# Kernel tuning notes

Measured on AMD Instinct MI355X. Metric: run time of the kernel, lower is better.

## Reference

```python
import jax, jax.numpy as jnp
import numpy as np

TEMPERATURE = 0.07
MASK_VALUE = -10000.0
EPS = 1e-12  # matches F.normalize eps


def setup_inputs() -> dict:
    key = jax.random.key(0)
    k1, k2 = jax.random.split(key)
    B, D = 8192, 512
    embeddings = jax.random.normal(k1, (B, D), dtype=jnp.float32)
    positive_mask = jax.random.randint(k2, (B, B), 0, 2).astype(bool)
    return {"embeddings": embeddings, "positive_mask": positive_mask}


def reference(embeddings, positive_mask):
    B = embeddings.shape[0]
    # L2 normalize rows (F.normalize with eps clamp)
    norm = jnp.maximum(jnp.linalg.norm(embeddings, axis=1, keepdims=True), EPS)
    e = embeddings / norm
    sim = jnp.matmul(e, e.T) / TEMPERATURE  # (B, B)
    eye = jnp.eye(B, dtype=bool)
    sim = jnp.where(eye, MASK_VALUE, sim)
    pos = positive_mask & ~eye
    counts = pos.sum(axis=1)  # (B,)
    pos_sum = jnp.sum(jnp.where(pos, sim, 0.0), axis=1)  # (B,)
    lse = jax.nn.logsumexp(sim, axis=1)  # (B,)
    pos_mean = pos_sum / jnp.maximum(counts, 1).astype(sim.dtype)
    # rows with positives: -mean(pos) + lse; rows without: just lse
    row_loss = jnp.where(counts > 0, lse - pos_mean, lse)
    return jnp.mean(row_loss)
```

## Files before the change

### kernel.cpp

```cpp
#include <hip/hip_runtime.h>
#include <hip/hip_bf16.h>

#define BN_ 8192
#define DK_ 512
#define TEMP_INV 14.2857142857142857f
#define LOG2E_ 1.44269504088896f
#define MAXOFF 15.0f

typedef __bf16 bf16x8 __attribute__((ext_vector_type(8)));
typedef float f32x4 __attribute__((ext_vector_type(4)));

__device__ inline unsigned short f2bf(float f) {
    unsigned u = __float_as_uint(f);
    return (unsigned short)((u + 0x7FFFu + ((u >> 16) & 1u)) >> 16);
}

__global__ __launch_bounds__(256) void norm_kernel(const float* __restrict__ emb,
                                                   unsigned short* __restrict__ ebf) {
    const int row  = blockIdx.x * 4 + (threadIdx.x >> 6);
    const int lane = threadIdx.x & 63;
    const float4* src = reinterpret_cast<const float4*>(emb + (size_t)row * DK_);
    float4 v0 = src[lane];
    float4 v1 = src[lane + 64];
    float ss = v0.x*v0.x + v0.y*v0.y + v0.z*v0.z + v0.w*v0.w
             + v1.x*v1.x + v1.y*v1.y + v1.z*v1.z + v1.w*v1.w;
#pragma unroll
    for (int off = 1; off < 64; off <<= 1) ss += __shfl_xor(ss, off, 64);
    const float scale = 1.0f / fmaxf(sqrtf(ss), 1e-12f);
    uint2 o0, o1;
    o0.x = (unsigned)f2bf(v0.x * scale) | ((unsigned)f2bf(v0.y * scale) << 16);
    o0.y = (unsigned)f2bf(v0.z * scale) | ((unsigned)f2bf(v0.w * scale) << 16);
    o1.x = (unsigned)f2bf(v1.x * scale) | ((unsigned)f2bf(v1.y * scale) << 16);
    o1.y = (unsigned)f2bf(v1.z * scale) | ((unsigned)f2bf(v1.w * scale) << 16);
    uint2* dst = reinterpret_cast<uint2*>(ebf + (size_t)row * DK_);
    dst[lane]      = o0;
    dst[lane + 64] = o1;
}

__global__ __launch_bounds__(256, 4) void infonce_main(
    const unsigned short* __restrict__ ebf,
    const int* __restrict__ mask,
    float* __restrict__ se, float* __restrict__ ps, float* __restrict__ ct) {

    __shared__ unsigned short As[128 * 64];
    __shared__ unsigned short Bs[128 * 64];
    __shared__ unsigned char  pmB[128 * 16];
    __shared__ float red2[2][128];

    const int t    = threadIdx.x;
    const int lane = t & 63;
    const int wid  = t >> 6;
    const int wr   = wid >> 1;
    const int wc   = wid & 1;
    const int rb   = blockIdx.x;
    const int cb   = blockIdx.y;

    if (t < 128) { red2[0][t] = 0.f; red2[1][t] = 0.f; }

    f32x4 acc[4][4] = {};

    const int sr  = t >> 3;
    const int scs = (((t & 7) ^ (sr & 7)) * 8);
    const size_t arow0 = (size_t)(rb * 128 + sr) * DK_ + scs;
    const size_t brow0 = (size_t)(cb * 128 + sr) * DK_ + scs;

    const int mr = t >> 4;
    const int mc = t & 15;
    const int* mbase = mask + (size_t)(rb * 128 + mr) * BN_ + cb * 128 + mc * 8;

    const int r16 = lane & 15;
    const int g4  = lane >> 4;
    const int r7  = r16 & 7;

#define STAGE(kt)                                                                          \
    {                                                                                      \
        const int k0_ = (kt) * 64;                                                         \
        _Pragma("unroll")                                                                  \
        for (int s = 0; s < 4; ++s) {                                                      \
            __builtin_amdgcn_global_load_lds(                                              \
                (const __attribute__((address_space(1))) void*)(ebf + arow0 + (size_t)s * 32 * DK_ + k0_), \
                (__attribute__((address_space(3))) void*)(As + s * 2048 + t * 8),          \
                16, 0, 0);                                                                 \
        }                                                                                  \
        _Pragma("unroll")                                                                  \
        for (int s = 0; s < 4; ++s) {                                                      \
            __builtin_amdgcn_global_load_lds(                                              \
                (const __attribute__((address_space(1))) void*)(ebf + brow0 + (size_t)s * 32 * DK_ + k0_), \
                (__attribute__((address_space(3))) void*)(Bs + s * 2048 + t * 8),          \
                16, 0, 0);                                                                 \
        }                                                                                  \
    }

    int4 m0[2], m1[2];

    { const int4* p = reinterpret_cast<const int4*>(mbase); m0[0] = p[0]; m1[0] = p[1]; }
    asm volatile("" ::: "memory");

#pragma unroll
    for (int kt = 0; kt < 8; ++kt) {
        STAGE(kt);
        asm volatile("" ::: "memory");
        if (kt < 7) {
            const int4* p = reinterpret_cast<const int4*>(mbase + (size_t)(kt + 1) * 16 * BN_);
            m0[(kt + 1) & 1] = p[0];
            m1[(kt + 1) & 1] = p[1];
        }
        asm volatile("" ::: "memory");
        if (kt < 7) { asm volatile("s_waitcnt vmcnt(2)" ::: "memory"); }
        else        { asm volatile("s_waitcnt vmcnt(0)" ::: "memory"); }
        __builtin_amdgcn_s_barrier();
        __builtin_amdgcn_sched_barrier(0);

        {
            const int4 a = m0[kt & 1], b = m1[kt & 1];
            unsigned by = (unsigned)(a.x != 0)        | ((unsigned)(a.y != 0) << 1)
                        | ((unsigned)(a.z != 0) << 2) | ((unsigned)(a.w != 0) << 3)
                        | ((unsigned)(b.x != 0) << 4) | ((unsigned)(b.y != 0) << 5)
                        | ((unsigned)(b.z != 0) << 6) | ((unsigned)(b.w != 0) << 7);
            pmB[(kt * 16 + mr) * 16 + mc] = (unsigned char)by;
        }

#pragma unroll
        for (int ks = 0; ks < 2; ++ks) {
            bf16x8 af[4], bfr[4];
            const int koff = (((ks * 4 + g4) ^ r7) * 8);
#pragma unroll
            for (int fm = 0; fm < 4; ++fm)
                af[fm] = *reinterpret_cast<const bf16x8*>(As + (wr * 64 + fm * 16 + r16) * 64 + koff);
#pragma unroll
            for (int fn = 0; fn < 4; ++fn)
                bfr[fn] = *reinterpret_cast<const bf16x8*>(Bs + (wc * 64 + fn * 16 + r16) * 64 + koff);
#pragma unroll
            for (int fm = 0; fm < 4; ++fm)
#pragma unroll
                for (int fn = 0; fn < 4; ++fn)
                    acc[fm][fn] = __builtin_amdgcn_mfma_f32_16x16x32_bf16(bfr[fn], af[fm], acc[fm][fn], 0, 0, 0);
        }
        __builtin_amdgcn_sched_barrier(0);
        __builtin_amdgcn_s_barrier();
        __builtin_amdgcn_sched_barrier(0);
    }
#undef STAGE
    __syncthreads();

    const float C1 = TEMP_INV * LOG2E_;
    const float C2 = -MAXOFF * LOG2E_;
    const bool  db  = (rb == cb);
    const int   gq4 = (lane >> 4) * 4;

#pragma unroll
    for (int fm = 0; fm < 4; ++fm) {
        const int li = wr * 64 + fm * 16 + (lane & 15);
        const uint4 rv = *reinterpret_cast<const uint4*>(pmB + li * 16);
        const unsigned w0 = wc ? rv.z : rv.x;
        const unsigned w1 = wc ? rv.w : rv.y;
        float lsep = 0.f, posp = 0.f;
#pragma unroll
        for (int fn = 0; fn < 4; ++fn) {
            const unsigned wsel = (fn < 2) ? w0 : w1;
#pragma unroll
            for (int rg = 0; rg < 4; ++rg) {
                const float a = acc[fm][fn][rg];
                const bool dg = db && (wr == wc) && (fm == fn) && ((lane & 15) == gq4 + rg);
                const float ex = dg ? 0.0f : exp2f(fmaf(a, C1, C2));
                lsep += ex;
                const bool p = (((wsel >> ((fn & 1) * 16 + gq4 + rg)) & 1u) != 0u) && !dg;
                posp += p ? a : 0.0f;
            }
        }
        lsep += __shfl_xor(lsep, 16, 64); lsep += __shfl_xor(lsep, 32, 64);
        posp += __shfl_xor(posp, 16, 64); posp += __shfl_xor(posp, 32, 64);
        if ((lane >> 4) == 0) {
            atomicAdd(&red2[0][li], lsep);
            atomicAdd(&red2[1][li], posp * TEMP_INV);
        }
    }
    __syncthreads();
    if (t < 128) {
        const uint4 rv = *reinterpret_cast<const uint4*>(pmB + t * 16);
        float cnt = (float)(__popc(rv.x) + __popc(rv.y) + __popc(rv.z) + __popc(rv.w));
        if (db) {
            const unsigned wsel = (t < 64) ? ((t < 32) ? rv.x : rv.y)
                                           : ((t < 96) ? rv.z : rv.w);
            cnt -= (float)((wsel >> (t & 31)) & 1u);
        }
        const int i = rb * 128 + t;
        atomicAdd(&se[i], red2[0][t]);
        atomicAdd(&ps[i], red2[1][t]);
        atomicAdd(&ct[i], cnt);
    }
}

__global__ __launch_bounds__(256) void finalize_kernel(const float* __restrict__ se,
                                                       const float* __restrict__ ps,
                                                       const float* __restrict__ ct,
                                                       float* __restrict__ out) {
    __shared__ float red[256];
    const int t = threadIdx.x;
    const int i = blockIdx.x * 256 + t;
    const float lse = logf(se[i]) + MAXOFF;
    red[t] = lse - ps[i] / fmaxf(ct[i], 1.0f);
    __syncthreads();
    for (int s = 128; s > 0; s >>= 1) {
        if (t < s) red[t] += red[t + s];
        __syncthreads();
    }
    if (t == 0) atomicAdd(out, red[0] * (1.0f / (float)BN_));
}

extern "C" void kernel_launch(void* const* d_in, const int* in_sizes, int n_in,
                              void* d_out, int out_size, void* d_ws, size_t ws_size,
                              hipStream_t stream) {
    const float* emb  = (const float*)d_in[0];
    const int*   mask = (const int*)d_in[1];
    float* out = (float*)d_out;

    char* ws = (char*)d_ws;
    unsigned short* ebf = (unsigned short*)ws;
    float* se = (float*)(ws + (size_t)8 * 1024 * 1024);
    float* ps = se + BN_;
    float* ct = ps + BN_;

    hipMemsetAsync(se, 0, (size_t)3 * BN_ * sizeof(float), stream);
    hipMemsetAsync(out, 0, sizeof(float), stream);
    norm_kernel<<<BN_ / 4, 256, 0, stream>>>(emb, ebf);
    infonce_main<<<dim3(64, 64), 256, 0, stream>>>(ebf, mask, se, ps, ct);
    finalize_kernel<<<BN_ / 256, 256, 0, stream>>>(se, ps, ct, out);
}
```

Measured before the change: 116.5 us.

## Switch similarity GEMM from bf16 to fp8 e4m3 MFMA with repacked layout

Normalized embeddings are now quantized to fp8 (e4m3, software rounding) instead of bf16, halving the operand bytes loaded into LDS. The main kernel uses fp8 16x16x32 MFMAs, with a new LDS swizzle and a permuted K layout written by the norm kernel. The aim is to cut GEMM compute and load cost. In exchange, the similarity values lose precision, amplified by the 1/0.07 temperature, which risks tolerance failures.

Result: slower. 161.5 us (+38.6%).

```diff
diff --git a/kernel.cpp b/kernel.cpp
--- a/kernel.cpp
+++ b/kernel.cpp
@@ -7,44 +7,53 @@
 #define LOG2E_ 1.44269504088896f
 #define MAXOFF 15.0f
 
-typedef __bf16 bf16x8 __attribute__((ext_vector_type(8)));
 typedef float f32x4 __attribute__((ext_vector_type(4)));
-
-__device__ inline unsigned short f2bf(float f) {
-    unsigned u = __float_as_uint(f);
-    return (unsigned short)((u + 0x7FFFu + ((u >> 16) & 1u)) >> 16);
+typedef long  lng2  __attribute__((ext_vector_type(2)));
+
+__device__ inline unsigned f2fp8(float f) {
+    const unsigned s = (__float_as_uint(f) >> 24) & 0x80u;
+    const float a = fabsf(f);
+    unsigned code;
+    if (a >= 0.015625f) {
+        unsigned u = __float_as_uint(a);
+        u += 0x7FFFFu + ((u >> 20) & 1u);
+        code = (((u >> 23) - 120u) << 3) | ((u >> 20) & 7u);
+    } else {
+        code = (unsigned)(int)(a * 512.0f + 0.5f);
+    }
+    return code | s;
 }
 
 __global__ __launch_bounds__(256) void norm_kernel(const float* __restrict__ emb,
-                                                   unsigned short* __restrict__ ebf) {
+                                                   unsigned char* __restrict__ e8) {
     const int row  = blockIdx.x * 4 + (threadIdx.x >> 6);
     const int lane = threadIdx.x & 63;
-    const float4* src = reinterpret_cast<const float4*>(emb + (size_t)row * DK_);
-    float4 v0 = src[lane];
-    float4 v1 = src[lane + 64];
-    float ss = v0.x*v0.x + v0.y*v0.y + v0.z*v0.z + v0.w*v0.w
-             + v1.x*v1.x + v1.y*v1.y + v1.z*v1.z + v1.w*v1.w;
+    const int kt = lane >> 3;
+    const int h  = lane & 1;
+    const int c  = (lane >> 1) & 3;
+    const int k0 = kt * 64 + h * 32 + c * 8;
+    const float* src = emb + (size_t)row * DK_ + k0;
+    float4 u0 = *reinterpret_cast<const float4*>(src);
+    float4 u1 = *reinterpret_cast<const float4*>(src + 4);
+    float ss = u0.x*u0.x + u0.y*u0.y + u0.z*u0.z + u0.w*u0.w
+             + u1.x*u1.x + u1.y*u1.y + u1.z*u1.z + u1.w*u1.w;
 #pragma unroll
     for (int off = 1; off < 64; off <<= 1) ss += __shfl_xor(ss, off, 64);
-    const float scale = 1.0f / fmaxf(sqrtf(ss), 1e-12f);
-    uint2 o0, o1;
-    o0.x = (unsigned)f2bf(v0.x * scale) | ((unsigned)f2bf(v0.y * scale) << 16);
-    o0.y = (unsigned)f2bf(v0.z * scale) | ((unsigned)f2bf(v0.w * scale) << 16);
-    o1.x = (unsigned)f2bf(v1.x * scale) | ((unsigned)f2bf(v1.y * scale) << 16);
-    o1.y = (unsigned)f2bf(v1.z * scale) | ((unsigned)f2bf(v1.w * scale) << 16);
-    uint2* dst = reinterpret_cast<uint2*>(ebf + (size_t)row * DK_);
-    dst[lane]      = o0;
-    dst[lane + 64] = o1;
+    const float sc = 1.0f / fmaxf(sqrtf(ss), 1e-12f);
+    uint2 o;
+    o.x = f2fp8(u0.x * sc) | (f2fp8(u0.y * sc) << 8) | (f2fp8(u0.z * sc) << 16) | (f2fp8(u0.w * sc) << 24);
+    o.y = f2fp8(u1.x * sc) | (f2fp8(u1.y * sc) << 8) | (f2fp8(u1.z * sc) << 16) | (f2fp8(u1.w * sc) << 24);
+    *reinterpret_cast<uint2*>(e8 + (size_t)row * 512 + lane * 8) = o;
 }
 
 __global__ __launch_bounds__(256, 4) void infonce_main(
-    const unsigned short* __restrict__ ebf,
+    const unsigned char* __restrict__ e8,
     const int* __restrict__ mask,
     float* __restrict__ se, float* __restrict__ ps, float* __restrict__ ct) {
 
-    __shared__ unsigned short As[128 * 64];
-    __shared__ unsigned short Bs[128 * 64];
-    __shared__ unsigned char  pmB[128 * 16];
+    __shared__ unsigned char As[128 * 64];
+    __shared__ unsigned char Bs[128 * 64];
+    __shared__ unsigned char pmB[128 * 16];
     __shared__ float red2[2][128];
 
     const int t    = threadIdx.x;
@@ -59,10 +68,10 @@
 
     f32x4 acc[4][4] = {};
 
-    const int sr  = t >> 3;
-    const int scs = (((t & 7) ^ (sr & 7)) * 8);
-    const size_t arow0 = (size_t)(rb * 128 + sr) * DK_ + scs;
-    const size_t brow0 = (size_t)(cb * 128 + sr) * DK_ + scs;
+    const int drow = t >> 2;
+    const int dchk = ((t & 3) ^ (drow & 3)) * 16;
+    const size_t asrc = (size_t)(rb * 128 + drow) * 512 + dchk;
+    const size_t bsrc = (size_t)(cb * 128 + drow) * 512 + dchk;
 
     const int mr = t >> 4;
     const int mc = t & 15;
@@ -70,23 +79,22 @@
 
     const int r16 = lane & 15;
     const int g4  = lane >> 4;
-    const int r7  = r16 & 7;
 
 #define STAGE(kt)                                                                          \
     {                                                                                      \
         const int k0_ = (kt) * 64;                                                         \
         _Pragma("unroll")                                                                  \
-        for (int s = 0; s < 4; ++s) {                                                      \
+        for (int s = 0; s < 2; ++s) {                                                      \
             __builtin_amdgcn_global_load_lds(                                              \
-                (const __attribute__((address_space(1))) void*)(ebf + arow0 + (size_t)s * 32 * DK_ + k0_), \
-                (__attribute__((address_space(3))) void*)(As + s * 2048 + t * 8),          \
+                (const __attribute__((address_space(1))) void*)(e8 + asrc + (size_t)s * 64 * 512 + k0_), \
+                (__attribute__((address_space(3))) void*)(As + s * 4096 + t * 16),         \
                 16, 0, 0);                                                                 \
         }                                                                                  \
         _Pragma("unroll")                                                                  \
-        for (int s = 0; s < 4; ++s) {                                                      \
+        for (int s = 0; s < 2; ++s) {                                                      \
             __builtin_amdgcn_global_load_lds(                                              \
-                (const __attribute__((address_space(1))) void*)(ebf + brow0 + (size_t)s * 32 * DK_ + k0_), \
-                (__attribute__((address_space(3))) void*)(Bs + s * 2048 + t * 8),          \
+                (const __attribute__((address_space(1))) void*)(e8 + bsrc + (size_t)s * 64 * 512 + k0_), \
+                (__attribute__((address_space(3))) void*)(Bs + s * 4096 + t * 16),         \
                 16, 0, 0);                                                                 \
         }                                                                                  \
     }
@@ -120,21 +128,23 @@
             pmB[(kt * 16 + mr) * 16 + mc] = (unsigned char)by;
         }
 
-#pragma unroll
-        for (int ks = 0; ks < 2; ++ks) {
-            bf16x8 af[4], bfr[4];
-            const int koff = (((ks * 4 + g4) ^ r7) * 8);
+        {
+            lng2 av[4], bv[4];
+            const int koff = ((g4 ^ (r16 & 3)) * 16);
 #pragma unroll
             for (int fm = 0; fm < 4; ++fm)
-                af[fm] = *reinterpret_cast<const bf16x8*>(As + (wr * 64 + fm * 16 + r16) * 64 + koff);
+                av[fm] = *reinterpret_cast<const lng2*>(As + (wr * 64 + fm * 16 + r16) * 64 + koff);
 #pragma unroll
             for (int fn = 0; fn < 4; ++fn)
-                bfr[fn] = *reinterpret_cast<const bf16x8*>(Bs + (wc * 64 + fn * 16 + r16) * 64 + koff);
-#pragma unroll
-            for (int fm = 0; fm < 4; ++fm)
-#pragma unroll
-                for (int fn = 0; fn < 4; ++fn)
-                    acc[fm][fn] = __builtin_amdgcn_mfma_f32_16x16x32_bf16(bfr[fn], af[fm], acc[fm][fn], 0, 0, 0);
+                bv[fn] = *reinterpret_cast<const lng2*>(Bs + (wc * 64 + fn * 16 + r16) * 64 + koff);
+#pragma unroll
+            for (int ks = 0; ks < 2; ++ks)
+#pragma unroll
+                for (int fm = 0; fm < 4; ++fm)
+#pragma unroll
+                    for (int fn = 0; fn < 4; ++fn)
+                        acc[fm][fn] = __builtin_amdgcn_mfma_f32_16x16x32_fp8_fp8(
+                            bv[fn][ks], av[fm][ks], acc[fm][fn], 0, 0, 0);
         }
         __builtin_amdgcn_sched_barrier(0);
         __builtin_amdgcn_s_barrier();
@@ -216,14 +226,14 @@
     float* out = (float*)d_out;
 
     char* ws = (char*)d_ws;
-    unsigned short* ebf = (unsigned short*)ws;
+    unsigned char* e8 = (unsigned char*)ws;
     float* se = (float*)(ws + (size_t)8 * 1024 * 1024);
     float* ps = se + BN_;
     float* ct = ps + BN_;
 
     hipMemsetAsync(se, 0, (size_t)3 * BN_ * sizeof(float), stream);
     hipMemsetAsync(out, 0, sizeof(float), stream);
-    norm_kernel<<<BN_ / 4, 256, 0, stream>>>(emb, ebf);
-    infonce_main<<<dim3(64, 64), 256, 0, stream>>>(ebf, mask, se, ps, ct);
+    norm_kernel<<<BN_ / 4, 256, 0, stream>>>(emb, e8);
+    infonce_main<<<dim3(64, 64), 256, 0, stream>>>(e8, mask, se, ps, ct);
     finalize_kernel<<<BN_ / 256, 256, 0, stream>>>(se, ps, ct, out);
 }
```

## Shrink row tile to 64 with four column warps and raise occupancy

Applied to the files above, without the earlier changes.

The row tile drops from 128 to 64 rows. The four warps now each own 32 columns of a 128-column tile instead of a 2x2 layout, so the grid doubles to 128x64 blocks. Mask bits are packed per nibble and merged through a shuffle. The diagonal and count logic is remapped for the half-height tile. Per-block LDS and registers shrink, which allows launch bounds of 6 blocks per CU, but B-operand reuse per block halves and embedding traffic rises.

Measured after the change: 158.8 us. 36.3% more time.

```diff
diff --git a/kernel.cpp b/kernel.cpp
--- a/kernel.cpp
+++ b/kernel.cpp
@@ -37,36 +37,34 @@
     dst[lane + 64] = o1;
 }
 
-__global__ __launch_bounds__(256, 4) void infonce_main(
+__global__ __launch_bounds__(256, 6) void infonce_main(
     const unsigned short* __restrict__ ebf,
     const int* __restrict__ mask,
     float* __restrict__ se, float* __restrict__ ps, float* __restrict__ ct) {
 
-    __shared__ unsigned short As[128 * 64];
+    __shared__ unsigned short As[64 * 64];
     __shared__ unsigned short Bs[128 * 64];
-    __shared__ unsigned char  pmB[128 * 16];
-    __shared__ float red2[2][128];
+    __shared__ unsigned char  pmB[64 * 16];
+    __shared__ float red2[2][64];
 
     const int t    = threadIdx.x;
     const int lane = t & 63;
-    const int wid  = t >> 6;
-    const int wr   = wid >> 1;
-    const int wc   = wid & 1;
+    const int wc   = t >> 6;
     const int rb   = blockIdx.x;
     const int cb   = blockIdx.y;
 
-    if (t < 128) { red2[0][t] = 0.f; red2[1][t] = 0.f; }
-
-    f32x4 acc[4][4] = {};
+    if (t < 64) { red2[0][t] = 0.f; red2[1][t] = 0.f; }
+
+    f32x4 acc[4][2] = {};
 
     const int sr  = t >> 3;
     const int scs = (((t & 7) ^ (sr & 7)) * 8);
-    const size_t arow0 = (size_t)(rb * 128 + sr) * DK_ + scs;
+    const size_t arow0 = (size_t)(rb * 64  + sr) * DK_ + scs;
     const size_t brow0 = (size_t)(cb * 128 + sr) * DK_ + scs;
 
-    const int mr = t >> 4;
-    const int mc = t & 15;
-    const int* mbase = mask + (size_t)(rb * 128 + mr) * BN_ + cb * 128 + mc * 8;
+    const int mr = t >> 5;
+    const int mc = t & 31;
+    const int* mbase = mask + (size_t)(rb * 64 + mr) * BN_ + cb * 128 + mc * 4;
 
     const int r16 = lane & 15;
     const int g4  = lane >> 4;
@@ -76,7 +74,7 @@
     {                                                                                      \
         const int k0_ = (kt) * 64;                                                         \
         _Pragma("unroll")                                                                  \
-        for (int s = 0; s < 4; ++s) {                                                      \
+        for (int s = 0; s < 2; ++s) {                                                      \
             __builtin_amdgcn_global_load_lds(                                              \
                 (const __attribute__((address_space(1))) void*)(ebf + arow0 + (size_t)s * 32 * DK_ + k0_), \
                 (__attribute__((address_space(3))) void*)(As + s * 2048 + t * 8),          \
@@ -91,9 +89,9 @@
         }                                                                                  \
     }
 
-    int4 m0[2], m1[2];
-
-    { const int4* p = reinterpret_cast<const int4*>(mbase); m0[0] = p[0]; m1[0] = p[1]; }
+    int4 m[2];
+
+    m[0] = *reinterpret_cast<const int4*>(mbase);
     asm volatile("" ::: "memory");
 
 #pragma unroll
@@ -101,39 +99,37 @@
         STAGE(kt);
         asm volatile("" ::: "memory");
         if (kt < 7) {
-            const int4* p = reinterpret_cast<const int4*>(mbase + (size_t)(kt + 1) * 16 * BN_);
-            m0[(kt + 1) & 1] = p[0];
-            m1[(kt + 1) & 1] = p[1];
+            m[(kt + 1) & 1] = *reinterpret_cast<const int4*>(mbase + (size_t)(kt + 1) * 8 * BN_);
         }
         asm volatile("" ::: "memory");
-        if (kt < 7) { asm volatile("s_waitcnt vmcnt(2)" ::: "memory"); }
+        if (kt < 7) { asm volatile("s_waitcnt vmcnt(1)" ::: "memory"); }
         else        { asm volatile("s_waitcnt vmcnt(0)" ::: "memory"); }
         __builtin_amdgcn_s_barrier();
         __builtin_amdgcn_sched_barrier(0);
 
         {
-            const int4 a = m0[kt & 1], b = m1[kt & 1];
-            unsigned by = (unsigned)(a.x != 0)        | ((unsigned)(a.y != 0) << 1)
-                        | ((unsigned)(a.z != 0) << 2) | ((unsigned)(a.w != 0) << 3)
-                        | ((unsigned)(b.x != 0) << 4) | ((unsigned)(b.y != 0) << 5)
-                        | ((unsigned)(b.z != 0) << 6) | ((unsigned)(b.w != 0) << 7);
-            pmB[(kt * 16 + mr) * 16 + mc] = (unsigned char)by;
+            const int4 a = m[kt & 1];
+            unsigned nib = (unsigned)(a.x != 0)        | ((unsigned)(a.y != 0) << 1)
+                         | ((unsigned)(a.z != 0) << 2) | ((unsigned)(a.w != 0) << 3);
+            const unsigned nib2 = __shfl_down(nib, 1, 64);
+            if ((lane & 1) == 0)
+                pmB[(kt * 8 + mr) * 16 + (mc >> 1)] = (unsigned char)(nib | (nib2 << 4));
         }
 
 #pragma unroll
         for (int ks = 0; ks < 2; ++ks) {
-            bf16x8 af[4], bfr[4];
+            bf16x8 af[4], bfr[2];
             const int koff = (((ks * 4 + g4) ^ r7) * 8);
 #pragma unroll
             for (int fm = 0; fm < 4; ++fm)
-                af[fm] = *reinterpret_cast<const bf16x8*>(As + (wr * 64 + fm * 16 + r16) * 64 + koff);
-#pragma unroll
-            for (int fn = 0; fn < 4; ++fn)
-                bfr[fn] = *reinterpret_cast<const bf16x8*>(Bs + (wc * 64 + fn * 16 + r16) * 64 + koff);
+                af[fm] = *reinterpret_cast<const bf16x8*>(As + (fm * 16 + r16) * 64 + koff);
+#pragma unroll
+            for (int fn = 0; fn < 2; ++fn)
+                bfr[fn] = *reinterpret_cast<const bf16x8*>(Bs + (wc * 32 + fn * 16 + r16) * 64 + koff);
 #pragma unroll
             for (int fm = 0; fm < 4; ++fm)
 #pragma unroll
-                for (int fn = 0; fn < 4; ++fn)
+                for (int fn = 0; fn < 2; ++fn)
                     acc[fm][fn] = __builtin_amdgcn_mfma_f32_16x16x32_bf16(bfr[fn], af[fm], acc[fm][fn], 0, 0, 0);
         }
         __builtin_amdgcn_sched_barrier(0);
@@ -145,26 +141,27 @@
 
     const float C1 = TEMP_INV * LOG2E_;
     const float C2 = -MAXOFF * LOG2E_;
-    const bool  db  = (rb == cb);
-    const int   gq4 = (lane >> 4) * 4;
+    const bool dbb = ((rb >> 1) == cb);
+    const int  dof = (rb & 1) << 6;
+    const int  l15 = lane & 15;
+    const int  gq4 = (lane >> 4) * 4;
 
 #pragma unroll
     for (int fm = 0; fm < 4; ++fm) {
-        const int li = wr * 64 + fm * 16 + (lane & 15);
+        const int li = fm * 16 + l15;
         const uint4 rv = *reinterpret_cast<const uint4*>(pmB + li * 16);
-        const unsigned w0 = wc ? rv.z : rv.x;
-        const unsigned w1 = wc ? rv.w : rv.y;
+        const unsigned w = (wc == 0) ? rv.x : (wc == 1) ? rv.y : (wc == 2) ? rv.z : rv.w;
         float lsep = 0.f, posp = 0.f;
 #pragma unroll
-        for (int fn = 0; fn < 4; ++fn) {
-            const unsigned wsel = (fn < 2) ? w0 : w1;
+        for (int fn = 0; fn < 2; ++fn) {
 #pragma unroll
             for (int rg = 0; rg < 4; ++rg) {
+                const int jl = wc * 32 + fn * 16 + gq4 + rg;
                 const float a = acc[fm][fn][rg];
-                const bool dg = db && (wr == wc) && (fm == fn) && ((lane & 15) == gq4 + rg);
+                const bool dg = dbb && (jl == dof + li);
                 const float ex = dg ? 0.0f : exp2f(fmaf(a, C1, C2));
                 lsep += ex;
-                const bool p = (((wsel >> ((fn & 1) * 16 + gq4 + rg)) & 1u) != 0u) && !dg;
+                const bool p = (((w >> (fn * 16 + gq4 + rg)) & 1u) != 0u) && !dg;
                 posp += p ? a : 0.0f;
             }
         }
@@ -176,15 +173,16 @@
         }
     }
     __syncthreads();
-    if (t < 128) {
+    if (t < 64) {
         const uint4 rv = *reinterpret_cast<const uint4*>(pmB + t * 16);
         float cnt = (float)(__popc(rv.x) + __popc(rv.y) + __popc(rv.z) + __popc(rv.w));
-        if (db) {
-            const unsigned wsel = (t < 64) ? ((t < 32) ? rv.x : rv.y)
-                                           : ((t < 96) ? rv.z : rv.w);
-            cnt -= (float)((wsel >> (t & 31)) & 1u);
-        }
-        const int i = rb * 128 + t;
+        if (dbb) {
+            const int d = dof + t;
+            const unsigned wsel = (d < 64) ? ((d < 32) ? rv.x : rv.y)
+                                           : ((d < 96) ? rv.z : rv.w);
+            cnt -= (float)((wsel >> (d & 31)) & 1u);
+        }
+        const int i = rb * 64 + t;
         atomicAdd(&se[i], red2[0][t]);
         atomicAdd(&ps[i], red2[1][t]);
         atomicAdd(&ct[i], cnt);
@@ -224,6 +222,6 @@
     hipMemsetAsync(se, 0, (size_t)3 * BN_ * sizeof(float), stream);
     hipMemsetAsync(out, 0, sizeof(float), stream);
     norm_kernel<<<BN_ / 4, 256, 0, stream>>>(emb, ebf);
-    infonce_main<<<dim3(64, 64), 256, 0, stream>>>(ebf, mask, se, ps, ct);
+    infonce_main<<<dim3(128, 64), 256, 0, stream>>>(ebf, mask, se, ps, ct);
     finalize_kernel<<<BN_ / 256, 256, 0, stream>>>(se, ps, ct, out);
 }
```
